# Optimization experiments

Measured on AMD Instinct MI355X. Metric: run time of the kernel, lower is better.

Reference implementation:

```python
import jax, jax.numpy as jnp
import numpy as np

B, N, HID, IN_NF, L = 32, 64, 128, 32, 4


def _w(k, shape):
    fan_in = shape[-2]
    return jax.random.normal(k, shape, jnp.float32) / np.sqrt(fan_in).astype(np.float32)


def setup_inputs() -> dict:
    key = jax.random.key(0)
    ks = jax.random.split(key, 12)
    n_nodes = B * N
    # fully connected edges within each graph, offset for flat batch layout
    r, c = np.meshgrid(np.arange(N), np.arange(N), indexing='ij')
    m = r != c
    r, c = r[m], c[m]                      # (N*(N-1),)
    offs = (np.arange(B) * N)[:, None]
    edge_row = jnp.asarray((r[None] + offs).reshape(-1), dtype=jnp.int32)
    edge_col = jnp.asarray((c[None] + offs).reshape(-1), dtype=jnp.int32)
    n_edges = edge_row.shape[0]            # 129024
    return {
        'h': jax.random.normal(ks[0], (n_nodes, IN_NF), jnp.float32),
        'x': jax.random.normal(ks[1], (n_nodes, 3), jnp.float32),
        'edge_row': edge_row,
        'edge_col': edge_col,
        'edge_attr': jax.random.normal(ks[2], (n_edges, HID), jnp.float32) * 0.1,
        'emb_w': _w(ks[3], (IN_NF, HID)), 'emb_b': jnp.zeros((HID,), jnp.float32),
        'edge_w1': _w(ks[4], (L, 3 * HID + 1, HID)), 'edge_b1': jnp.zeros((L, HID), jnp.float32),
        'edge_w2': _w(ks[5], (L, HID, HID)), 'edge_b2': jnp.zeros((L, HID), jnp.float32),
        'node_w1': _w(ks[6], (L, 2 * HID, HID)), 'node_b1': jnp.zeros((L, HID), jnp.float32),
        'node_w2': _w(ks[7], (L, HID, HID)), 'node_b2': jnp.zeros((L, HID), jnp.float32),
        'coord_w1': _w(ks[8], (L, HID, HID)), 'coord_b1': jnp.zeros((L, HID), jnp.float32),
        'coord_w2': jax.random.normal(ks[9], (L, HID, 1), jnp.float32) * 0.001,  # xavier gain=0.001, no bias
    }


def reference(h, x, edge_row, edge_col, edge_attr,
              emb_w, emb_b,
              edge_w1, edge_b1, edge_w2, edge_b2,
              node_w1, node_b1, node_w2, node_b2,
              coord_w1, coord_b1, coord_w2):
    n_nodes = h.shape[0]
    silu = jax.nn.silu
    # degree for 'mean' coordinate aggregation (segments guaranteed nonempty via clip)
    ones = jnp.ones((edge_row.shape[0], 1), h.dtype)
    deg = jnp.clip(jax.ops.segment_sum(ones, edge_row, num_segments=n_nodes), 1.0)
    h = h @ emb_w + emb_b  # embedding_in
    for i in range(L):
        diff = x[edge_row] - x[edge_col]                 # (E,3)
        radial = jnp.sum(diff * diff, axis=1, keepdims=True)  # (E,1)
        # edge model: MLP([h_i, h_j, radial, edge_attr])
        e_in = jnp.concatenate([h[edge_row], h[edge_col], radial, edge_attr], axis=1)
        m = silu(silu(e_in @ edge_w1[i] + edge_b1[i]) @ edge_w2[i] + edge_b2[i])  # (E,HID)
        # coord model: mean-aggregated weighted differences
        trans = diff * (silu(m @ coord_w1[i] + coord_b1[i]) @ coord_w2[i])
        x = x + jax.ops.segment_sum(trans, edge_row, num_segments=n_nodes) / deg
        # node model with residual
        agg = jax.ops.segment_sum(m, edge_row, num_segments=n_nodes)
        n_in = jnp.concatenate([h, agg], axis=1)
        h = h + (silu(n_in @ node_w1[i] + node_b1[i]) @ node_w2[i] + node_b2[i])
        edge_attr = m  # backbone re-feeds edge_feat as next layer's edge_attr
    return h  # (B*N, HID); node_mask is None -> raw node embeddings returned
```

## Files before the change

### kernel.cpp

```cpp
#include <hip/hip_runtime.h>
#include <cstdint>
#include <cstddef>

#define HID    128
#define K1     385
#define NLAYER 4
#define NNODES 2048
#define NEDGES 129024
#define DEG    63
#define EPB    64
#define EBLOCKS (NEDGES / EPB)
#define EA_STRIDE 256
#define NPB    32
#define NBLOCKS (NNODES / NPB)

#define EIN_STRIDE 512
#define MBASE   16384
#define REDBASE 32768
#define RADBASE 34816
#define HR1BASE 35072
#define ELDS    36096

typedef __attribute__((ext_vector_type(8))) short short8;
typedef __attribute__((ext_vector_type(4))) float f32x4;

__device__ __forceinline__ unsigned short f2bf(float f) {
    unsigned int u = __builtin_bit_cast(unsigned int, f);
    unsigned int r = u + 0x7fffu + ((u >> 16) & 1u);
    return (unsigned short)(r >> 16);
}
__device__ __forceinline__ float bf2f(unsigned short h) {
    unsigned int u = ((unsigned int)h) << 16;
    return __builtin_bit_cast(float, u);
}
__device__ __forceinline__ float silu_f(float v) {
    return v / (1.0f + __expf(-v));
}

__global__ __launch_bounds__(64) void pack_w_kernel(
    const float* __restrict__ src, unsigned short* __restrict__ dst,
    const int KK, const int layerStride, const int mode)
{
    int b = blockIdx.x;
    const int tn = b & 7; b >>= 3;
    const int kk = b % KK;
    const int layer = b / KK;
    const int lane = threadIdx.x, lq = lane >> 4, lr = lane & 15;
    const float* s = src + (size_t)layer * layerStride;
    unsigned short* d = dst + (size_t)layer * (KK * 8 * 64 * 8)
                            + ((size_t)(kk * 8 + tn) * 64 + lane) * 8;
#pragma unroll
    for (int j = 0; j < 8; ++j) {
        const int kd = kk * 32 + lq * 8 + j;
        const int ka = mode ? (128 + kd + (kd >= 128 ? 1 : 0)) : kd;
        d[j] = f2bf(s[(size_t)ka * HID + tn * 16 + lr]);
    }
}

__global__ __launch_bounds__(128) void embed_kernel(
    const float* __restrict__ h_in, const float* __restrict__ emb_w,
    const float* __restrict__ emb_b, const float* __restrict__ eW1,
    float* __restrict__ h_ws, unsigned short* __restrict__ h_bf,
    float* __restrict__ hr1, float* __restrict__ agg,
    const float* __restrict__ x_in, float* __restrict__ x_a)
{
    const int n = blockIdx.x;
    const int o = threadIdx.x;
    __shared__ float hin[32];
    __shared__ float hrow[HID];
    if (o < 32) hin[o] = h_in[n * 32 + o];
    __syncthreads();
    float acc = emb_b[o];
#pragma unroll
    for (int k = 0; k < 32; ++k) acc += hin[k] * emb_w[k * HID + o];
    h_ws[n * HID + o] = acc;
    h_bf[n * HID + o] = f2bf(acc);
    hrow[o] = acc;
    agg[n * HID + o] = 0.0f;
    if (o < 3) x_a[n * 3 + o] = x_in[n * 3 + o];
    __syncthreads();
    float a2 = 0.0f;
    for (int k = 0; k < HID; ++k) a2 += hrow[k] * eW1[k * HID + o];
    hr1[n * HID + o] = a2;
}

__global__ __launch_bounds__(512, 6) void edge_mfma_kernel(
    const unsigned short* __restrict__ h_bf, const float* __restrict__ x,
    const float* __restrict__ ea_f32, unsigned short* __restrict__ ea,
    const int first_layer, const float* __restrict__ hr1,
    const short8* __restrict__ w1p, const float* __restrict__ b1, const float* __restrict__ w256,
    const short8* __restrict__ w2p, const float* __restrict__ b2,
    const short8* __restrict__ cw1p, const float* __restrict__ cb1, const float* __restrict__ cw2,
    float* __restrict__ c_out, float* __restrict__ agg)
{
    __shared__ __align__(16) char smem[ELDS];
    float* red    = (float*)(smem + REDBASE);
    float* radial = (float*)(smem + RADBASE);
    float* hr1s   = (float*)(smem + HR1BASE);
    const int t = threadIdx.x;
    const int w = t >> 6, lane = t & 63, lq = lane >> 4, lr = lane & 15;
    const int ebase = blockIdx.x * EPB;
    const int n0 = ebase / DEG;
    const int esplit = DEG * (n0 + 1) - ebase;

    {
        const int s = t & 15, g = t >> 4;
#pragma unroll
        for (int j = 0; j < 2; ++j) {
            const int r = g + j * 32;
            const int e = ebase + r;
            const int row = n0 + (r >= esplit ? 1 : 0);
            const int jj = e - row * DEG;
            const int rl = row & 63;
            const int col = (row & ~63) + jj + (jj >= rl ? 1 : 0);
            const int swz = (r & 7) << 4;
            *(uint4*)(smem + r * EIN_STRIDE + ((s * 16) ^ swz)) =
                *(const uint4*)(h_bf + (size_t)col * HID + s * 8);
            uint4 v;
            if (first_layer) {
                const float4* ef = (const float4*)(ea_f32 + (size_t)e * HID);
                const float4 f0 = ef[s * 2], f1 = ef[s * 2 + 1];
                v.x = (unsigned)f2bf(f0.x) | ((unsigned)f2bf(f0.y) << 16);
                v.y = (unsigned)f2bf(f0.z) | ((unsigned)f2bf(f0.w) << 16);
                v.z = (unsigned)f2bf(f1.x) | ((unsigned)f2bf(f1.y) << 16);
                v.w = (unsigned)f2bf(f1.z) | ((unsigned)f2bf(f1.w) << 16);
            } else {
                v = *(const uint4*)(ea + (size_t)e * EA_STRIDE + s * 8);
            }
            *(uint4*)(smem + r * EIN_STRIDE + (((s + 16) * 16) ^ swz)) = v;
            if (s == 0) {
                const float dx = x[row * 3 + 0] - x[col * 3 + 0];
                const float dy = x[row * 3 + 1] - x[col * 3 + 1];
                const float dz = x[row * 3 + 2] - x[col * 3 + 2];
                radial[r] = dx * dx + dy * dy + dz * dz;
            }
        }
        if (t < 256) hr1s[t] = hr1[(size_t)(n0 + (t >> 7)) * HID + (t & 127)];
    }
    __syncthreads();

    const int c0 = w * 16 + lr;

    f32x4 acc1[4] = {};
#pragma unroll
    for (int kk = 0; kk < 8; ++kk) {
        const short8 bf = w1p[(kk * 8 + w) * 64 + lane];
#pragma unroll
        for (int mt = 0; mt < 4; ++mt) {
            const int r = mt * 16 + lr;
            const short8 af = *(const short8*)(smem + r * EIN_STRIDE +
                                ((kk * 64 + lq * 16) ^ ((r & 7) << 4)));
            acc1[mt] = __builtin_amdgcn_mfma_f32_16x16x32_bf16(af, bf, acc1[mt], 0, 0, 0);
        }
    }
    __syncthreads();

    {
        const float bb = b1[c0], ww = w256[c0];
        const float ha = hr1s[c0], hb = hr1s[128 + c0];
#pragma unroll
        for (int mt = 0; mt < 4; ++mt)
#pragma unroll
            for (int reg = 0; reg < 4; ++reg) {
                const int r = mt * 16 + lq * 4 + reg;
                const float v = silu_f(acc1[mt][reg] + bb + radial[r] * ww +
                                       (r < esplit ? ha : hb));
                *(unsigned short*)(smem + r * 256 + ((c0 * 2) ^ ((r & 7) << 4))) = f2bf(v);
            }
    }
    __syncthreads();

    f32x4 acc2[4] = {};
#pragma unroll
    for (int kk = 0; kk < 4; ++kk) {
        const short8 bf = w2p[(kk * 8 + w) * 64 + lane];
#pragma unroll
        for (int mt = 0; mt < 4; ++mt) {
            const int r = mt * 16 + lr;
            const short8 af = *(const short8*)(smem + r * 256 +
                                ((kk * 64 + lq * 16) ^ ((r & 7) << 4)));
            acc2[mt] = __builtin_amdgcn_mfma_f32_16x16x32_bf16(af, bf, acc2[mt], 0, 0, 0);
        }
    }
    {
        const float bb = b2[c0];
        float s0 = 0.0f, s1 = 0.0f;
#pragma unroll
        for (int mt = 0; mt < 4; ++mt)
#pragma unroll
            for (int reg = 0; reg < 4; ++reg) {
                const int r = mt * 16 + lq * 4 + reg;
                const float v = silu_f(acc2[mt][reg] + bb);
                if (r < esplit) s0 += v; else s1 += v;
                *(unsigned short*)(smem + MBASE + r * 256 + ((c0 * 2) ^ ((r & 7) << 4))) = f2bf(v);
            }
        s0 += __shfl_xor(s0, 16); s0 += __shfl_xor(s0, 32);
        s1 += __shfl_xor(s1, 16); s1 += __shfl_xor(s1, 32);
        if (lane < 16) {
            atomicAdd(&agg[(size_t)n0 * HID + c0], s0);
            atomicAdd(&agg[(size_t)(n0 + 1) * HID + c0], s1);
        }
    }
    __syncthreads();

    f32x4 acc3[4] = {};
#pragma unroll
    for (int kk = 0; kk < 4; ++kk) {
        const short8 bf = cw1p[(kk * 8 + w) * 64 + lane];
#pragma unroll
        for (int mt = 0; mt < 4; ++mt) {
            const int r = mt * 16 + lr;
            const short8 af = *(const short8*)(smem + MBASE + r * 256 +
                                ((kk * 64 + lq * 16) ^ ((r & 7) << 4)));
            acc3[mt] = __builtin_amdgcn_mfma_f32_16x16x32_bf16(af, bf, acc3[mt], 0, 0, 0);
        }
    }
    {
        const int s = t & 15, g = t >> 4;
#pragma unroll
        for (int j = 0; j < 2; ++j) {
            const int r = g + j * 32;
            const uint4 v = *(const uint4*)(smem + MBASE + r * 256 +
                                            ((s * 16) ^ ((r & 7) << 4)));
            *(uint4*)(ea + (size_t)(ebase + r) * EA_STRIDE + s * 8) = v;
        }
    }
    {
        const float cb = cb1[c0], wc = cw2[c0];
#pragma unroll
        for (int mt = 0; mt < 4; ++mt)
#pragma unroll
            for (int reg = 0; reg < 4; ++reg) {
                float p = silu_f(acc3[mt][reg] + cb) * wc;
                p += __shfl_xor(p, 1);
                p += __shfl_xor(p, 2);
                p += __shfl_xor(p, 4);
                p += __shfl_xor(p, 8);
                if (lr == 0) red[w * 64 + mt * 16 + lq * 4 + reg] = p;
            }
    }
    __syncthreads();
    if (t < 64) {
        float s = 0.0f;
#pragma unroll
        for (int ww = 0; ww < 8; ++ww) s += red[ww * 64 + t];
        c_out[ebase + t] = s;
    }
}

__global__ __launch_bounds__(512, 4) void node_mfma_kernel(
    float* __restrict__ h_ws, unsigned short* __restrict__ h_bf,
    float* __restrict__ agg,
    const short8* __restrict__ nw1p, const float* __restrict__ nb1,
    const short8* __restrict__ nw2p, const float* __restrict__ nb2,
    const short8* __restrict__ w1a_next, float* __restrict__ hr1,
    const float* __restrict__ x_in, float* __restrict__ x_out,
    const float* __restrict__ c_ws,
    float* __restrict__ out, const int write_out, const int do_coord)
{
    __shared__ __align__(16) char smem[32768];
    const int t = threadIdx.x;
    const int w = t >> 6, lane = t & 63, lq = lane >> 4, lr = lane & 15;
    const int nb = blockIdx.x * NPB;

    {
        const int s = t & 15, g = t >> 4;
        const int node = nb + g;
        const int swz = (g & 7) << 4;
        *(uint4*)(smem + g * 512 + ((s * 16) ^ swz)) =
            *(const uint4*)(h_bf + (size_t)node * HID + s * 8);
        float4* agg4 = (float4*)(agg + (size_t)node * HID);
        const float4 a0 = agg4[s * 2], a1 = agg4[s * 2 + 1];
        agg4[s * 2] = float4{0, 0, 0, 0};
        agg4[s * 2 + 1] = float4{0, 0, 0, 0};
        uint4 v;
        v.x = (unsigned)f2bf(a0.x) | ((unsigned)f2bf(a0.y) << 16);
        v.y = (unsigned)f2bf(a0.z) | ((unsigned)f2bf(a0.w) << 16);
        v.z = (unsigned)f2bf(a1.x) | ((unsigned)f2bf(a1.y) << 16);
        v.w = (unsigned)f2bf(a1.z) | ((unsigned)f2bf(a1.w) << 16);
        *(uint4*)(smem + g * 512 + (((s + 16) * 16) ^ swz)) = v;
    }
    __syncthreads();

    const int c0 = w * 16 + lr;

    f32x4 acc1[2] = {};
#pragma unroll
    for (int kk = 0; kk < 8; ++kk) {
        const short8 bf = nw1p[(kk * 8 + w) * 64 + lane];
#pragma unroll
        for (int mt = 0; mt < 2; ++mt) {
            const int r = mt * 16 + lr;
            const short8 af = *(const short8*)(smem + r * 512 +
                                ((kk * 64 + lq * 16) ^ ((r & 7) << 4)));
            acc1[mt] = __builtin_amdgcn_mfma_f32_16x16x32_bf16(af, bf, acc1[mt], 0, 0, 0);
        }
    }
    __syncthreads();
    {
        const float bb = nb1[c0];
#pragma unroll
        for (int mt = 0; mt < 2; ++mt)
#pragma unroll
            for (int reg = 0; reg < 4; ++reg) {
                const int r = mt * 16 + lq * 4 + reg;
                const float v = silu_f(acc1[mt][reg] + bb);
                *(unsigned short*)(smem + 16384 + r * 256 + ((c0 * 2) ^ ((r & 7) << 4))) = f2bf(v);
            }
    }
    __syncthreads();
    f32x4 acc2[2] = {};
#pragma unroll
    for (int kk = 0; kk < 4; ++kk) {
        const short8 bf = nw2p[(kk * 8 + w) * 64 + lane];
#pragma unroll
        for (int mt = 0; mt < 2; ++mt) {
            const int r = mt * 16 + lr;
            const short8 af = *(const short8*)(smem + 16384 + r * 256 +
                                ((kk * 64 + lq * 16) ^ ((r & 7) << 4)));
            acc2[mt] = __builtin_amdgcn_mfma_f32_16x16x32_bf16(af, bf, acc2[mt], 0, 0, 0);
        }
    }
    {
        const float bb = nb2[c0];
#pragma unroll
        for (int mt = 0; mt < 2; ++mt)
#pragma unroll
            for (int reg = 0; reg < 4; ++reg) {
                const int r = mt * 16 + lq * 4 + reg;
                const size_t gi = (size_t)(nb + r) * HID + c0;
                const float hnew = h_ws[gi] + acc2[mt][reg] + bb;
                h_ws[gi] = hnew;
                h_bf[gi] = f2bf(hnew);
                if (write_out) out[gi] = hnew;
                *(unsigned short*)(smem + 24576 + r * 256 + ((c0 * 2) ^ ((r & 7) << 4))) = f2bf(hnew);
            }
    }
    __syncthreads();
    if (w1a_next) {
        f32x4 acch[2] = {};
#pragma unroll
        for (int kk = 0; kk < 4; ++kk) {
            const short8 bf = w1a_next[(kk * 8 + w) * 64 + lane];
#pragma unroll
            for (int mt = 0; mt < 2; ++mt) {
                const int r = mt * 16 + lr;
                const short8 af = *(const short8*)(smem + 24576 + r * 256 +
                                    ((kk * 64 + lq * 16) ^ ((r & 7) << 4)));
                acch[mt] = __builtin_amdgcn_mfma_f32_16x16x32_bf16(af, bf, acch[mt], 0, 0, 0);
            }
        }
#pragma unroll
        for (int mt = 0; mt < 2; ++mt)
#pragma unroll
            for (int reg = 0; reg < 4; ++reg) {
                const int r = mt * 16 + lq * 4 + reg;
                hr1[(size_t)(nb + r) * HID + c0] = acch[mt][reg];
            }
    }
    if (do_coord) {
        const int nl = t >> 4, sub = t & 15;
        const int n = nb + nl;
        const int rl = n & 63, base = n & ~63;
        const float xi0 = x_in[n * 3 + 0], xi1 = x_in[n * 3 + 1], xi2 = x_in[n * 3 + 2];
        float p0 = 0, p1 = 0, p2 = 0;
#pragma unroll
        for (int kk = 0; kk < 4; ++kk) {
            const int k = sub + kk * 16;
            if (k < DEG) {
                const int e = n * DEG + k;
                const int col = base + k + (k >= rl ? 1 : 0);
                const float c = c_ws[e];
                p0 += c * (xi0 - x_in[col * 3 + 0]);
                p1 += c * (xi1 - x_in[col * 3 + 1]);
                p2 += c * (xi2 - x_in[col * 3 + 2]);
            }
        }
#pragma unroll
        for (int off = 1; off < 16; off <<= 1) {
            p0 += __shfl_xor(p0, off);
            p1 += __shfl_xor(p1, off);
            p2 += __shfl_xor(p2, off);
        }
        if (sub == 0) {
            const float inv = 1.0f / DEG;
            x_out[n * 3 + 0] = xi0 + p0 * inv;
            x_out[n * 3 + 1] = xi1 + p1 * inv;
            x_out[n * 3 + 2] = xi2 + p2 * inv;
        }
    }
}

extern "C" void kernel_launch(void* const* d_in, const int* in_sizes, int n_in,
                              void* d_out, int out_size, void* d_ws, size_t ws_size,
                              hipStream_t stream)
{
    const float* h_in  = (const float*)d_in[0];
    const float* x_in  = (const float*)d_in[1];
    const float* ea0   = (const float*)d_in[4];
    const float* emb_w = (const float*)d_in[5];
    const float* emb_b = (const float*)d_in[6];
    const float* eW1   = (const float*)d_in[7];
    const float* eB1   = (const float*)d_in[8];
    const float* eW2   = (const float*)d_in[9];
    const float* eB2   = (const float*)d_in[10];
    const float* nW1   = (const float*)d_in[11];
    const float* nB1   = (const float*)d_in[12];
    const float* nW2   = (const float*)d_in[13];
    const float* nB2   = (const float*)d_in[14];
    const float* cW1   = (const float*)d_in[15];
    const float* cB1   = (const float*)d_in[16];
    const float* cW2   = (const float*)d_in[17];
    float* out = (float*)d_out;

    unsigned short* ea_bf = (unsigned short*)d_in[4];

    char* p = (char*)d_ws;
    float* h_ws = (float*)p;                    p += (size_t)NNODES * HID * 4;
    unsigned short* h_bf = (unsigned short*)p;  p += (size_t)NNODES * HID * 2;
    float* agg  = (float*)p;                    p += (size_t)NNODES * HID * 4;
    float* hr1  = (float*)p;                    p += (size_t)NNODES * HID * 4;
    float* x_a  = (float*)p;                    p += NNODES * 3 * 4 + 16;
    float* x_b  = (float*)p;                    p += NNODES * 3 * 4 + 16;
    float* c_ws = (float*)p;                    p += (size_t)NEDGES * 4;
    unsigned short* w1p  = (unsigned short*)p;  p += (size_t)NLAYER * 8 * 8 * 64 * 8 * 2;
    unsigned short* w1a  = (unsigned short*)p;  p += (size_t)NLAYER * 4 * 8 * 64 * 8 * 2;
    unsigned short* w2p  = (unsigned short*)p;  p += (size_t)NLAYER * 4 * 8 * 64 * 8 * 2;
    unsigned short* cw1p = (unsigned short*)p;  p += (size_t)NLAYER * 4 * 8 * 64 * 8 * 2;
    unsigned short* nw1p = (unsigned short*)p;  p += (size_t)NLAYER * 8 * 8 * 64 * 8 * 2;
    unsigned short* nw2p = (unsigned short*)p;  p += (size_t)NLAYER * 4 * 8 * 64 * 8 * 2;

    const int SL8 = 8 * 8 * 64 * 8;
    const int SL4 = 4 * 8 * 64 * 8;

    pack_w_kernel<<<NLAYER * 8 * 8, 64, 0, stream>>>(eW1, w1p, 8, K1 * HID, 1);
    pack_w_kernel<<<NLAYER * 4 * 8, 64, 0, stream>>>(eW1, w1a, 4, K1 * HID, 0);
    pack_w_kernel<<<NLAYER * 4 * 8, 64, 0, stream>>>(eW2, w2p, 4, HID * HID, 0);
    pack_w_kernel<<<NLAYER * 4 * 8, 64, 0, stream>>>(cW1, cw1p, 4, HID * HID, 0);
    pack_w_kernel<<<NLAYER * 8 * 8, 64, 0, stream>>>(nW1, nw1p, 8, 2 * HID * HID, 0);
    pack_w_kernel<<<NLAYER * 4 * 8, 64, 0, stream>>>(nW2, nw2p, 4, HID * HID, 0);

    embed_kernel<<<NNODES, HID, 0, stream>>>(h_in, emb_w, emb_b, eW1,
                                             h_ws, h_bf, hr1, agg, x_in, x_a);

    float* xc = x_a;
    float* xn = x_b;
    for (int i = 0; i < NLAYER; ++i) {
        edge_mfma_kernel<<<EBLOCKS, 512, 0, stream>>>(
            h_bf, xc, ea0, ea_bf, (i == 0) ? 1 : 0, hr1,
            (const short8*)(w1p + (size_t)i * SL8), eB1 + i * HID,
            eW1 + ((size_t)i * K1 + 256) * HID,
            (const short8*)(w2p + (size_t)i * SL4), eB2 + i * HID,
            (const short8*)(cw1p + (size_t)i * SL4), cB1 + i * HID,
            cW2 + (size_t)i * HID, c_ws, agg);
        node_mfma_kernel<<<NBLOCKS, 512, 0, stream>>>(
            h_ws, h_bf, agg,
            (const short8*)(nw1p + (size_t)i * SL8), nB1 + i * HID,
            (const short8*)(nw2p + (size_t)i * SL4), nB2 + i * HID,
            (i < NLAYER - 1) ? (const short8*)(w1a + (size_t)(i + 1) * SL4) : (const short8*)nullptr,
            hr1, xc, xn, c_ws,
            out, (i == NLAYER - 1) ? 1 : 0, (i < NLAYER - 1) ? 1 : 0);
        float* tmp = xc; xc = xn; xn = tmp;
    }
}
```

Measured before the change: 369.4 us.

## Merge weight packing, fold edge bias into hr1, restructure coord MLP and halve node tile

Merges the six weight-packing launches into one kernel and folds the edge first-layer bias into the precomputed per-node hr1 term. The coordinate MLP is rewritten so each wave owns an edge tile and reduces over hidden units in registers, with coord bias and weights staged in LDS, which cuts the cross-wave LDS reduction. Node blocks drop from 32 to 16 nodes, doubling the block count and shrinking LDS. It also switches to hardware packed bf16 conversion and a reciprocal-based silu. The trade-off is less weight reuse per node block and slightly different rounding.

```diff
diff --git a/kernel.cpp b/kernel.cpp
--- a/kernel.cpp
+++ b/kernel.cpp
@@ -11,42 +11,54 @@
 #define EPB    64
 #define EBLOCKS (NEDGES / EPB)
 #define EA_STRIDE 256
-#define NPB    32
+#define NPB    16
 #define NBLOCKS (NNODES / NPB)
 
 #define EIN_STRIDE 512
 #define MBASE   16384
 #define REDBASE 32768
-#define RADBASE 34816
-#define HR1BASE 35072
-#define ELDS    36096
+#define RADBASE 33280
+#define HR1BASE 33536
+#define CB1BASE 34560
+#define CW2BASE 35072
+#define ELDS    35584
 
 typedef __attribute__((ext_vector_type(8))) short short8;
 typedef __attribute__((ext_vector_type(4))) float f32x4;
 
-__device__ __forceinline__ unsigned short f2bf(float f) {
-    unsigned int u = __builtin_bit_cast(unsigned int, f);
-    unsigned int r = u + 0x7fffu + ((u >> 16) & 1u);
-    return (unsigned short)(r >> 16);
-}
-__device__ __forceinline__ float bf2f(unsigned short h) {
-    unsigned int u = ((unsigned int)h) << 16;
-    return __builtin_bit_cast(float, u);
+__device__ __forceinline__ unsigned pkbf(float a, float b) {
+    unsigned r;
+    asm("v_cvt_pk_bf16_f32 %0, %1, %2" : "=v"(r) : "v"(a), "v"(b));
+    return r;
+}
+__device__ __forceinline__ unsigned short f2bf(float a) {
+    return (unsigned short)pkbf(a, a);
 }
 __device__ __forceinline__ float silu_f(float v) {
-    return v / (1.0f + __expf(-v));
-}
-
-__global__ __launch_bounds__(64) void pack_w_kernel(
-    const float* __restrict__ src, unsigned short* __restrict__ dst,
-    const int KK, const int layerStride, const int mode)
+    return v * __builtin_amdgcn_rcpf(1.0f + __expf(-v));
+}
+
+__global__ __launch_bounds__(64) void pack_all_kernel(
+    const float* __restrict__ eW1, const float* __restrict__ eW2,
+    const float* __restrict__ cW1, const float* __restrict__ nW1,
+    const float* __restrict__ nW2,
+    unsigned short* __restrict__ w1p, unsigned short* __restrict__ w1a,
+    unsigned short* __restrict__ w2p, unsigned short* __restrict__ cw1p,
+    unsigned short* __restrict__ nw1p, unsigned short* __restrict__ nw2p)
 {
     int b = blockIdx.x;
+    const float* src; unsigned short* dst; int KK, ls, mode;
+    if (b < 256)      { src = eW1; dst = w1p;  KK = 8; ls = K1 * HID;      mode = 1; }
+    else if (b < 384) { src = eW1; dst = w1a;  KK = 4; ls = K1 * HID;      mode = 0; b -= 256; }
+    else if (b < 512) { src = eW2; dst = w2p;  KK = 4; ls = HID * HID;     mode = 0; b -= 384; }
+    else if (b < 640) { src = cW1; dst = cw1p; KK = 4; ls = HID * HID;     mode = 0; b -= 512; }
+    else if (b < 896) { src = nW1; dst = nw1p; KK = 8; ls = 2 * HID * HID; mode = 0; b -= 640; }
+    else              { src = nW2; dst = nw2p; KK = 4; ls = HID * HID;     mode = 0; b -= 896; }
     const int tn = b & 7; b >>= 3;
     const int kk = b % KK;
     const int layer = b / KK;
     const int lane = threadIdx.x, lq = lane >> 4, lr = lane & 15;
-    const float* s = src + (size_t)layer * layerStride;
+    const float* s = src + (size_t)layer * ls;
     unsigned short* d = dst + (size_t)layer * (KK * 8 * 64 * 8)
                             + ((size_t)(kk * 8 + tn) * 64 + lane) * 8;
 #pragma unroll
@@ -60,6 +72,7 @@
 __global__ __launch_bounds__(128) void embed_kernel(
     const float* __restrict__ h_in, const float* __restrict__ emb_w,
     const float* __restrict__ emb_b, const float* __restrict__ eW1,
+    const float* __restrict__ eB1,
     float* __restrict__ h_ws, unsigned short* __restrict__ h_bf,
     float* __restrict__ hr1, float* __restrict__ agg,
     const float* __restrict__ x_in, float* __restrict__ x_a)
@@ -79,7 +92,7 @@
     agg[n * HID + o] = 0.0f;
     if (o < 3) x_a[n * 3 + o] = x_in[n * 3 + o];
     __syncthreads();
-    float a2 = 0.0f;
+    float a2 = eB1[o];
     for (int k = 0; k < HID; ++k) a2 += hrow[k] * eW1[k * HID + o];
     hr1[n * HID + o] = a2;
 }
@@ -88,7 +101,7 @@
     const unsigned short* __restrict__ h_bf, const float* __restrict__ x,
     const float* __restrict__ ea_f32, unsigned short* __restrict__ ea,
     const int first_layer, const float* __restrict__ hr1,
-    const short8* __restrict__ w1p, const float* __restrict__ b1, const float* __restrict__ w256,
+    const short8* __restrict__ w1p, const float* __restrict__ w256,
     const short8* __restrict__ w2p, const float* __restrict__ b2,
     const short8* __restrict__ cw1p, const float* __restrict__ cb1, const float* __restrict__ cw2,
     float* __restrict__ c_out, float* __restrict__ agg)
@@ -97,6 +110,8 @@
     float* red    = (float*)(smem + REDBASE);
     float* radial = (float*)(smem + RADBASE);
     float* hr1s   = (float*)(smem + HR1BASE);
+    float* cb1s   = (float*)(smem + CB1BASE);
+    float* cw2s   = (float*)(smem + CW2BASE);
     const int t = threadIdx.x;
     const int w = t >> 6, lane = t & 63, lq = lane >> 4, lr = lane & 15;
     const int ebase = blockIdx.x * EPB;
@@ -120,10 +135,10 @@
             if (first_layer) {
                 const float4* ef = (const float4*)(ea_f32 + (size_t)e * HID);
                 const float4 f0 = ef[s * 2], f1 = ef[s * 2 + 1];
-                v.x = (unsigned)f2bf(f0.x) | ((unsigned)f2bf(f0.y) << 16);
-                v.y = (unsigned)f2bf(f0.z) | ((unsigned)f2bf(f0.w) << 16);
-                v.z = (unsigned)f2bf(f1.x) | ((unsigned)f2bf(f1.y) << 16);
-                v.w = (unsigned)f2bf(f1.z) | ((unsigned)f2bf(f1.w) << 16);
+                v.x = pkbf(f0.x, f0.y);
+                v.y = pkbf(f0.z, f0.w);
+                v.z = pkbf(f1.x, f1.y);
+                v.w = pkbf(f1.z, f1.w);
             } else {
                 v = *(const uint4*)(ea + (size_t)e * EA_STRIDE + s * 8);
             }
@@ -135,7 +150,11 @@
                 radial[r] = dx * dx + dy * dy + dz * dz;
             }
         }
-        if (t < 256) hr1s[t] = hr1[(size_t)(n0 + (t >> 7)) * HID + (t & 127)];
+        if (t < 128) { cb1s[t] = cb1[t]; cw2s[t] = cw2[t]; }
+        else if (t < 384) {
+            const int i2 = t - 128;
+            hr1s[i2] = hr1[(size_t)(n0 + (i2 >> 7)) * HID + (i2 & 127)];
+        }
     }
     __syncthreads();
 
@@ -156,14 +175,14 @@
     __syncthreads();
 
     {
-        const float bb = b1[c0], ww = w256[c0];
+        const float ww = w256[c0];
         const float ha = hr1s[c0], hb = hr1s[128 + c0];
 #pragma unroll
         for (int mt = 0; mt < 4; ++mt)
 #pragma unroll
             for (int reg = 0; reg < 4; ++reg) {
                 const int r = mt * 16 + lq * 4 + reg;
-                const float v = silu_f(acc1[mt][reg] + bb + radial[r] * ww +
+                const float v = silu_f(acc1[mt][reg] + radial[r] * ww +
                                        (r < esplit ? ha : hb));
                 *(unsigned short*)(smem + r * 256 + ((c0 * 2) ^ ((r & 7) << 4))) = f2bf(v);
             }
@@ -203,16 +222,20 @@
     }
     __syncthreads();
 
+    const int etile = w & 3, jhalf = w >> 2;
     f32x4 acc3[4] = {};
-#pragma unroll
-    for (int kk = 0; kk < 4; ++kk) {
-        const short8 bf = cw1p[(kk * 8 + w) * 64 + lane];
-#pragma unroll
-        for (int mt = 0; mt < 4; ++mt) {
-            const int r = mt * 16 + lr;
-            const short8 af = *(const short8*)(smem + MBASE + r * 256 +
-                                ((kk * 64 + lq * 16) ^ ((r & 7) << 4)));
-            acc3[mt] = __builtin_amdgcn_mfma_f32_16x16x32_bf16(af, bf, acc3[mt], 0, 0, 0);
+    {
+        const int erow = etile * 16 + lr;
+        const int eswz = (erow & 7) << 4;
+#pragma unroll
+        for (int kb = 0; kb < 4; ++kb) {
+            const short8 mf = *(const short8*)(smem + MBASE + erow * 256 +
+                                ((kb * 64 + lq * 16) ^ eswz));
+#pragma unroll
+            for (int jt = 0; jt < 4; ++jt) {
+                const short8 af = cw1p[(kb * 8 + jhalf * 4 + jt) * 64 + lane];
+                acc3[jt] = __builtin_amdgcn_mfma_f32_16x16x32_bf16(af, mf, acc3[jt], 0, 0, 0);
+            }
         }
     }
     {
@@ -226,26 +249,20 @@
         }
     }
     {
-        const float cb = cb1[c0], wc = cw2[c0];
-#pragma unroll
-        for (int mt = 0; mt < 4; ++mt)
+        float p = 0.0f;
+#pragma unroll
+        for (int jt = 0; jt < 4; ++jt)
 #pragma unroll
             for (int reg = 0; reg < 4; ++reg) {
-                float p = silu_f(acc3[mt][reg] + cb) * wc;
-                p += __shfl_xor(p, 1);
-                p += __shfl_xor(p, 2);
-                p += __shfl_xor(p, 4);
-                p += __shfl_xor(p, 8);
-                if (lr == 0) red[w * 64 + mt * 16 + lq * 4 + reg] = p;
-            }
-    }
-    __syncthreads();
-    if (t < 64) {
-        float s = 0.0f;
-#pragma unroll
-        for (int ww = 0; ww < 8; ++ww) s += red[ww * 64 + t];
-        c_out[ebase + t] = s;
-    }
+                const int j2 = jhalf * 64 + jt * 16 + lq * 4 + reg;
+                p += silu_f(acc3[jt][reg] + cb1s[j2]) * cw2s[j2];
+            }
+        p += __shfl_xor(p, 16);
+        p += __shfl_xor(p, 32);
+        if (lane < 16) red[jhalf * 64 + etile * 16 + lane] = p;
+    }
+    __syncthreads();
+    if (t < 64) c_out[ebase + t] = red[t] + red[64 + t];
 }
 
 __global__ __launch_bounds__(512, 4) void node_mfma_kernel(
@@ -253,120 +270,108 @@
     float* __restrict__ agg,
     const short8* __restrict__ nw1p, const float* __restrict__ nb1,
     const short8* __restrict__ nw2p, const float* __restrict__ nb2,
-    const short8* __restrict__ w1a_next, float* __restrict__ hr1,
+    const short8* __restrict__ w1a_next, const float* __restrict__ b1_next,
+    float* __restrict__ hr1,
     const float* __restrict__ x_in, float* __restrict__ x_out,
     const float* __restrict__ c_ws,
     float* __restrict__ out, const int write_out, const int do_coord)
 {
-    __shared__ __align__(16) char smem[32768];
+    __shared__ __align__(16) char smem[16384];
     const int t = threadIdx.x;
     const int w = t >> 6, lane = t & 63, lq = lane >> 4, lr = lane & 15;
     const int nb = blockIdx.x * NPB;
 
     {
-        const int s = t & 15, g = t >> 4;
+        const int s = t & 31, g = t >> 5;
         const int node = nb + g;
         const int swz = (g & 7) << 4;
-        *(uint4*)(smem + g * 512 + ((s * 16) ^ swz)) =
-            *(const uint4*)(h_bf + (size_t)node * HID + s * 8);
-        float4* agg4 = (float4*)(agg + (size_t)node * HID);
-        const float4 a0 = agg4[s * 2], a1 = agg4[s * 2 + 1];
-        agg4[s * 2] = float4{0, 0, 0, 0};
-        agg4[s * 2 + 1] = float4{0, 0, 0, 0};
-        uint4 v;
-        v.x = (unsigned)f2bf(a0.x) | ((unsigned)f2bf(a0.y) << 16);
-        v.y = (unsigned)f2bf(a0.z) | ((unsigned)f2bf(a0.w) << 16);
-        v.z = (unsigned)f2bf(a1.x) | ((unsigned)f2bf(a1.y) << 16);
-        v.w = (unsigned)f2bf(a1.z) | ((unsigned)f2bf(a1.w) << 16);
-        *(uint4*)(smem + g * 512 + (((s + 16) * 16) ^ swz)) = v;
+        if (s < 16) {
+            *(uint4*)(smem + g * 512 + ((s * 16) ^ swz)) =
+                *(const uint4*)(h_bf + (size_t)node * HID + s * 8);
+        } else {
+            const int q = s - 16;
+            float4* agg4 = (float4*)(agg + (size_t)node * HID);
+            const float4 a0 = agg4[q * 2], a1 = agg4[q * 2 + 1];
+            agg4[q * 2]     = float4{0, 0, 0, 0};
+            agg4[q * 2 + 1] = float4{0, 0, 0, 0};
+            uint4 v;
+            v.x = pkbf(a0.x, a0.y);
+            v.y = pkbf(a0.z, a0.w);
+            v.z = pkbf(a1.x, a1.y);
+            v.w = pkbf(a1.z, a1.w);
+            *(uint4*)(smem + g * 512 + ((s * 16) ^ swz)) = v;
+        }
     }
     __syncthreads();
 
     const int c0 = w * 16 + lr;
 
-    f32x4 acc1[2] = {};
+    f32x4 acc1 = {};
 #pragma unroll
     for (int kk = 0; kk < 8; ++kk) {
         const short8 bf = nw1p[(kk * 8 + w) * 64 + lane];
-#pragma unroll
-        for (int mt = 0; mt < 2; ++mt) {
-            const int r = mt * 16 + lr;
-            const short8 af = *(const short8*)(smem + r * 512 +
-                                ((kk * 64 + lq * 16) ^ ((r & 7) << 4)));
-            acc1[mt] = __builtin_amdgcn_mfma_f32_16x16x32_bf16(af, bf, acc1[mt], 0, 0, 0);
-        }
+        const short8 af = *(const short8*)(smem + lr * 512 +
+                            ((kk * 64 + lq * 16) ^ ((lr & 7) << 4)));
+        acc1 = __builtin_amdgcn_mfma_f32_16x16x32_bf16(af, bf, acc1, 0, 0, 0);
     }
     __syncthreads();
     {
         const float bb = nb1[c0];
 #pragma unroll
-        for (int mt = 0; mt < 2; ++mt)
-#pragma unroll
-            for (int reg = 0; reg < 4; ++reg) {
-                const int r = mt * 16 + lq * 4 + reg;
-                const float v = silu_f(acc1[mt][reg] + bb);
-                *(unsigned short*)(smem + 16384 + r * 256 + ((c0 * 2) ^ ((r & 7) << 4))) = f2bf(v);
-            }
-    }
-    __syncthreads();
-    f32x4 acc2[2] = {};
+        for (int reg = 0; reg < 4; ++reg) {
+            const int r = lq * 4 + reg;
+            const float v = silu_f(acc1[reg] + bb);
+            *(unsigned short*)(smem + 8192 + r * 256 + ((c0 * 2) ^ ((r & 7) << 4))) = f2bf(v);
+        }
+    }
+    __syncthreads();
+    f32x4 acc2 = {};
 #pragma unroll
     for (int kk = 0; kk < 4; ++kk) {
         const short8 bf = nw2p[(kk * 8 + w) * 64 + lane];
-#pragma unroll
-        for (int mt = 0; mt < 2; ++mt) {
-            const int r = mt * 16 + lr;
-            const short8 af = *(const short8*)(smem + 16384 + r * 256 +
-                                ((kk * 64 + lq * 16) ^ ((r & 7) << 4)));
-            acc2[mt] = __builtin_amdgcn_mfma_f32_16x16x32_bf16(af, bf, acc2[mt], 0, 0, 0);
-        }
+        const short8 af = *(const short8*)(smem + 8192 + lr * 256 +
+                            ((kk * 64 + lq * 16) ^ ((lr & 7) << 4)));
+        acc2 = __builtin_amdgcn_mfma_f32_16x16x32_bf16(af, bf, acc2, 0, 0, 0);
     }
     {
         const float bb = nb2[c0];
 #pragma unroll
-        for (int mt = 0; mt < 2; ++mt)
-#pragma unroll
-            for (int reg = 0; reg < 4; ++reg) {
-                const int r = mt * 16 + lq * 4 + reg;
-                const size_t gi = (size_t)(nb + r) * HID + c0;
-                const float hnew = h_ws[gi] + acc2[mt][reg] + bb;
-                h_ws[gi] = hnew;
-                h_bf[gi] = f2bf(hnew);
-                if (write_out) out[gi] = hnew;
-                *(unsigned short*)(smem + 24576 + r * 256 + ((c0 * 2) ^ ((r & 7) << 4))) = f2bf(hnew);
-            }
+        for (int reg = 0; reg < 4; ++reg) {
+            const int r = lq * 4 + reg;
+            const size_t gi = (size_t)(nb + r) * HID + c0;
+            const float hnew = h_ws[gi] + acc2[reg] + bb;
+            h_ws[gi] = hnew;
+            h_bf[gi] = f2bf(hnew);
+            if (write_out) out[gi] = hnew;
+            *(unsigned short*)(smem + 12288 + r * 256 + ((c0 * 2) ^ ((r & 7) << 4))) = f2bf(hnew);
+        }
     }
     __syncthreads();
     if (w1a_next) {
-        f32x4 acch[2] = {};
+        f32x4 acch = {};
 #pragma unroll
         for (int kk = 0; kk < 4; ++kk) {
             const short8 bf = w1a_next[(kk * 8 + w) * 64 + lane];
-#pragma unroll
-            for (int mt = 0; mt < 2; ++mt) {
-                const int r = mt * 16 + lr;
-                const short8 af = *(const short8*)(smem + 24576 + r * 256 +
-                                    ((kk * 64 + lq * 16) ^ ((r & 7) << 4)));
-                acch[mt] = __builtin_amdgcn_mfma_f32_16x16x32_bf16(af, bf, acch[mt], 0, 0, 0);
-            }
-        }
-#pragma unroll
-        for (int mt = 0; mt < 2; ++mt)
-#pragma unroll
-            for (int reg = 0; reg < 4; ++reg) {
-                const int r = mt * 16 + lq * 4 + reg;
-                hr1[(size_t)(nb + r) * HID + c0] = acch[mt][reg];
-            }
+            const short8 af = *(const short8*)(smem + 12288 + lr * 256 +
+                                ((kk * 64 + lq * 16) ^ ((lr & 7) << 4)));
+            acch = __builtin_amdgcn_mfma_f32_16x16x32_bf16(af, bf, acch, 0, 0, 0);
+        }
+        const float bb = b1_next[c0];
+#pragma unroll
+        for (int reg = 0; reg < 4; ++reg) {
+            const int r = lq * 4 + reg;
+            hr1[(size_t)(nb + r) * HID + c0] = acch[reg] + bb;
+        }
     }
     if (do_coord) {
-        const int nl = t >> 4, sub = t & 15;
+        const int nl = t >> 5, sub = t & 31;
         const int n = nb + nl;
         const int rl = n & 63, base = n & ~63;
         const float xi0 = x_in[n * 3 + 0], xi1 = x_in[n * 3 + 1], xi2 = x_in[n * 3 + 2];
         float p0 = 0, p1 = 0, p2 = 0;
 #pragma unroll
-        for (int kk = 0; kk < 4; ++kk) {
-            const int k = sub + kk * 16;
+        for (int kk = 0; kk < 2; ++kk) {
+            const int k = sub + kk * 32;
             if (k < DEG) {
                 const int e = n * DEG + k;
                 const int col = base + k + (k >= rl ? 1 : 0);
@@ -377,7 +382,7 @@
             }
         }
 #pragma unroll
-        for (int off = 1; off < 16; off <<= 1) {
+        for (int off = 1; off < 32; off <<= 1) {
             p0 += __shfl_xor(p0, off);
             p1 += __shfl_xor(p1, off);
             p2 += __shfl_xor(p2, off);
@@ -433,14 +438,10 @@
     const int SL8 = 8 * 8 * 64 * 8;
     const int SL4 = 4 * 8 * 64 * 8;
 
-    pack_w_kernel<<<NLAYER * 8 * 8, 64, 0, stream>>>(eW1, w1p, 8, K1 * HID, 1);
-    pack_w_kernel<<<NLAYER * 4 * 8, 64, 0, stream>>>(eW1, w1a, 4, K1 * HID, 0);
-    pack_w_kernel<<<NLAYER * 4 * 8, 64, 0, stream>>>(eW2, w2p, 4, HID * HID, 0);
-    pack_w_kernel<<<NLAYER * 4 * 8, 64, 0, stream>>>(cW1, cw1p, 4, HID * HID, 0);
-    pack_w_kernel<<<NLAYER * 8 * 8, 64, 0, stream>>>(nW1, nw1p, 8, 2 * HID * HID, 0);
-    pack_w_kernel<<<NLAYER * 4 * 8, 64, 0, stream>>>(nW2, nw2p, 4, HID * HID, 0);
-
-    embed_kernel<<<NNODES, HID, 0, stream>>>(h_in, emb_w, emb_b, eW1,
+    pack_all_kernel<<<1024, 64, 0, stream>>>(eW1, eW2, cW1, nW1, nW2,
+                                             w1p, w1a, w2p, cw1p, nw1p, nw2p);
+
+    embed_kernel<<<NNODES, HID, 0, stream>>>(h_in, emb_w, emb_b, eW1, eB1,
                                              h_ws, h_bf, hr1, agg, x_in, x_a);
 
     float* xc = x_a;
@@ -448,7 +449,7 @@
     for (int i = 0; i < NLAYER; ++i) {
         edge_mfma_kernel<<<EBLOCKS, 512, 0, stream>>>(
             h_bf, xc, ea0, ea_bf, (i == 0) ? 1 : 0, hr1,
-            (const short8*)(w1p + (size_t)i * SL8), eB1 + i * HID,
+            (const short8*)(w1p + (size_t)i * SL8),
             eW1 + ((size_t)i * K1 + 256) * HID,
             (const short8*)(w2p + (size_t)i * SL4), eB2 + i * HID,
             (const short8*)(cw1p + (size_t)i * SL4), cB1 + i * HID,
@@ -458,6 +459,7 @@
             (const short8*)(nw1p + (size_t)i * SL8), nB1 + i * HID,
             (const short8*)(nw2p + (size_t)i * SL4), nB2 + i * HID,
             (i < NLAYER - 1) ? (const short8*)(w1a + (size_t)(i + 1) * SL4) : (const short8*)nullptr,
+            (i < NLAYER - 1) ? (eB1 + (size_t)(i + 1) * HID) : nullptr,
             hr1, xc, xn, c_ws,
             out, (i == NLAYER - 1) ? 1 : 0, (i < NLAYER - 1) ? 1 : 0);
         float* tmp = xc; xc = xn; xn = tmp;
```

After: 306.2 us. 17.1% less time.
